# Kernel tuning notes

Hardware: AMD Instinct MI355X
Metric: run time of the kernel (lower is better)

Reference implementation:

```python
import jax, jax.numpy as jnp
import numpy as np

H_IN, W_IN = 512, 896          # input_shape
H, W = 64, 224                 # current_shape = (h, w_expand // 6)
N_CAM = 6
NPF = 256                      # num_pos_feats
TEMP = 10000.0


def setup_inputs():
    key = jax.random.key(0)
    k0, k1, k2, k3, k4, k5 = jax.random.split(key, 6)
    b, n = 8, N_CAM
    # extrinsic: 4x4 with a near-orthonormal rotation block and translation (cam height ~1.5m)
    rot = jnp.eye(3) + 0.1 * jax.random.normal(k0, (b, n, 3, 3), dtype=jnp.float32)
    trans = jax.random.normal(k1, (b, n, 3), dtype=jnp.float32)
    trans = trans.at[..., 2].set(1.5 + 0.1 * jnp.abs(trans[..., 2]))
    extrinsic = jnp.zeros((b, n, 4, 4), dtype=jnp.float32)
    extrinsic = extrinsic.at[:, :, :3, :3].set(rot)
    extrinsic = extrinsic.at[:, :, :3, 3].set(trans)
    extrinsic = extrinsic.at[:, :, 3, 3].set(1.0)
    # intrinsic: pinhole K = [[fx,0,cx],[0,fy,cy],[0,0,1]] (well conditioned, invertible)
    fx = 800.0 + 50.0 * jax.random.normal(k2, (b, n), dtype=jnp.float32)
    fy = 800.0 + 50.0 * jax.random.normal(k3, (b, n), dtype=jnp.float32)
    cx = jnp.full((b, n), W_IN / 2.0, dtype=jnp.float32)
    cy = jnp.full((b, n), H_IN / 2.0, dtype=jnp.float32)
    intrinsic = jnp.zeros((b, n, 3, 3), dtype=jnp.float32)
    intrinsic = intrinsic.at[:, :, 0, 0].set(fx).at[:, :, 1, 1].set(fy)
    intrinsic = intrinsic.at[:, :, 0, 2].set(cx).at[:, :, 1, 2].set(cy)
    intrinsic = intrinsic.at[:, :, 2, 2].set(1.0)
    # ida (image data augmentation) matrices: scale + shift affine, invertible
    s = 0.5 + 0.05 * jax.random.uniform(k4, (b, n), dtype=jnp.float32)
    t = 10.0 * jax.random.normal(k5, (b, n, 2), dtype=jnp.float32)
    ida = jnp.zeros((b, n, 3, 3), dtype=jnp.float32)
    ida = ida.at[:, :, 0, 0].set(s).at[:, :, 1, 1].set(s)
    ida = ida.at[:, :, 0, 2].set(t[..., 0]).at[:, :, 1, 2].set(t[..., 1])
    ida = ida.at[:, :, 2, 2].set(1.0)
    return {"extrinsic": extrinsic, "intrinsic": intrinsic, "ida_mats": ida, "do_flip": 0}


def reference(extrinsic, intrinsic, ida_mats, do_flip):
    b, n = extrinsic.shape[0], extrinsic.shape[1]
    # pixel grid over the full input image, sampled at feature resolution
    x = jnp.linspace(0.0, W_IN - 1, W, dtype=jnp.float32)
    y = jnp.linspace(0.0, H_IN - 1, H, dtype=jnp.float32)
    yg, xg = jnp.meshgrid(y, x, indexing="ij")            # (H, W)
    coords = jnp.stack([xg, yg, jnp.ones_like(xg)], -1)    # (H, W, 3) homogeneous
    # combined per-camera 3x3: R @ K^{-1} @ ida^{-1}
    M = jnp.einsum("bnij,bnjk->bnik", jnp.linalg.inv(intrinsic), jnp.linalg.inv(ida_mats))
    RM = jnp.einsum("bnij,bnjk->bnik", extrinsic[:, :, :3, :3], M)
    world = jnp.einsum("bnij,hwj->bnhwi", RM, coords)      # (b, n, H, W, 3)
    # F.normalize(p=2, dim=-1): x / max(||x||, eps)
    norm = jnp.maximum(jnp.linalg.norm(world, axis=-1, keepdims=True), 1e-12)
    world = world / norm
    z = world[..., 2]
    trans_z = extrinsic[:, :, 2, 3][:, :, None, None]      # (b, n, 1, 1)
    depth = -trans_z / z
    valid = (depth > 0)[..., None]                          # (b, n, H, W, 1)
    xy = world[..., :2] * depth[..., None]                  # (b, n, H, W, 2)
    if do_flip:
        xy = xy * jnp.array([1.0, -1.0], dtype=xy.dtype)
    # cat(unbind(dim=1), dim=-2): stitch cameras along width -> (b, H, n*W, ...)
    xy = jnp.transpose(xy, (0, 2, 1, 3, 4)).reshape(b, H, n * W, 2)
    valid = jnp.transpose(valid, (0, 2, 1, 3, 4)).reshape(b, H, n * W, 1)
    # sine encoding
    half = NPF // 2
    d = jnp.arange(half, dtype=jnp.float32)
    dim_t = TEMP ** (2.0 * jnp.floor(d / 2.0) / half)       # (half,)
    p = xy[..., None] / dim_t                               # (b, H, nW, 2, half)
    px = jnp.stack([jnp.sin(p[..., 0, 0::2]), jnp.cos(p[..., 0, 1::2])], -1).reshape(b, H, n * W, half)
    py = jnp.stack([jnp.sin(p[..., 1, 0::2]), jnp.cos(p[..., 1, 1::2])], -1).reshape(b, H, n * W, half)
    pos = jnp.concatenate([py, px], axis=-1)                # (b, H, nW, NPF)
    pos = jnp.where(valid, pos, jnp.float32(0.0))
    pos = jnp.transpose(pos, (0, 3, 1, 2))                  # (b, NPF, H, nW)
    return pos, valid[..., 0]
```

## Files before the change

### kernel.cpp

```cpp
#include <hip/hip_runtime.h>
#include <math.h>

namespace {
constexpr int B    = 8;
constexpr int NCAM = 6;
constexpr int H    = 64;
constexpr int W    = 224;
constexpr int NW   = NCAM * W;
constexpr int NPF  = 256;
constexpr int WP4  = NW / 4;
constexpr long long POS_ELEMS = (long long)B * NPF * H * NW;
}

__device__ __forceinline__ void inv3(const float m[9], float o[9]) {
  float a = m[0], b = m[1], c = m[2];
  float d = m[3], e = m[4], f = m[5];
  float g = m[6], h = m[7], i = m[8];
  float A  =  e * i - f * h;
  float Bm = -(d * i - f * g);
  float C  =  d * h - e * g;
  float det = a * A + b * Bm + c * C;
  float r = 1.0f / det;
  o[0] = A * r;  o[1] = -(b * i - c * h) * r; o[2] =  (b * f - c * e) * r;
  o[3] = Bm * r; o[4] =  (a * i - c * g) * r; o[5] = -(a * f - c * d) * r;
  o[6] = C * r;  o[7] = -(a * h - b * g) * r; o[8] =  (a * e - b * d) * r;
}

__device__ __forceinline__ void mm3(const float* a, const float* bm, float* o) {
#pragma unroll
  for (int i = 0; i < 3; ++i) {
#pragma unroll
    for (int j = 0; j < 3; ++j) {
      o[i * 3 + j] = fmaf(a[i * 3 + 0], bm[0 * 3 + j],
                     fmaf(a[i * 3 + 1], bm[1 * 3 + j],
                          a[i * 3 + 2] * bm[2 * 3 + j]));
    }
  }
}

__global__ __launch_bounds__(256) void ipm_pos_kernel(
    const float* __restrict__ ext, const float* __restrict__ intr,
    const float* __restrict__ ida, const int* __restrict__ do_flip,
    float* __restrict__ out, int write_valid) {
  const int t   = blockIdx.x * blockDim.x + threadIdx.x;
  const int wp4 = t % WP4;
  const int bh  = t / WP4;
  const int h   = bh % H;
  const int b   = bh / H;
  if (b >= B) return;
  const int wp0 = wp4 * 4;
  const int cam = wp0 / W;

  const int mi = b * NCAM + cam;
  const float* E  = ext  + mi * 16;
  const float* Km = intr + mi * 9;
  const float* Am = ida  + mi * 9;

  float R[9] = {E[0], E[1], E[2], E[4], E[5], E[6], E[8], E[9], E[10]};
  const float tz = E[11];
  float K[9], A[9];
#pragma unroll
  for (int i = 0; i < 9; ++i) { K[i] = Km[i]; A[i] = Am[i]; }

  float Ki[9], Ai[9], M[9], RM[9];
  inv3(K, Ki);
  inv3(A, Ai);
  mm3(Ki, Ai, M);
  mm3(R, M, RM);

  const float yp   = (float)h * (511.0f / 63.0f);
  const int   flip = *do_flip;

  float X[4], Y[4], vmask[4];
#pragma unroll
  for (int p = 0; p < 4; ++p) {
    const int w = wp0 + p - cam * W;
    const float xp = (float)w * (895.0f / 223.0f);
    float wx = fmaf(RM[0], xp, fmaf(RM[1], yp, RM[2]));
    float wy = fmaf(RM[3], xp, fmaf(RM[4], yp, RM[5]));
    float wz = fmaf(RM[6], xp, fmaf(RM[7], yp, RM[8]));
    float norm = sqrtf(wx * wx + wy * wy + wz * wz);
    norm = fmaxf(norm, 1e-12f);
    const float nz = wz / norm;
    const float depth = -tz / nz;
    const bool valid = depth > 0.0f;
    float Xp = (wx / norm) * depth;
    float Yp = (wy / norm) * depth;
    if (flip) Yp = -Yp;
    X[p] = valid ? Xp : 0.0f;
    Y[p] = valid ? Yp : 0.0f;
    vmask[p] = valid ? 1.0f : 0.0f;
  }
  const float amax = fmaxf(fmaxf(fabsf(X[0]), fabsf(X[1])),
                           fmaxf(fabsf(X[2]), fabsf(X[3])));
  const float amay = fmaxf(fmaxf(fabsf(Y[0]), fabsf(Y[1])),
                           fmaxf(fabsf(Y[2]), fabsf(Y[3])));
  const float ama  = fmaxf(amax, amay);

  const float c1     = 0.2076205059304498f;
  const float INV2PI = 0.15915494309189535f;
  const size_t cs  = (size_t)H * NW;
  const size_t o00 = ((size_t)b * NPF * H + h) * NW + wp0;

  for (int k = 0; k < 64; ++k) {
    const float inv_t = exp2f((float)(-k) * c1);
    float4 vsy, vcy, vsx, vcx;
    float sy[4], cy[4], sx[4], cx[4];
    if (__builtin_expect(!__any(ama * inv_t > 800.0f), 1)) {
      const float ck = inv_t * INV2PI;
#pragma unroll
      for (int p = 0; p < 4; ++p) {
        const float ry = Y[p] * ck;
        const float rx = X[p] * ck;
        sy[p] = __builtin_amdgcn_sinf(ry);
        cy[p] = __builtin_amdgcn_cosf(ry);
        sx[p] = __builtin_amdgcn_sinf(rx);
        cx[p] = __builtin_amdgcn_cosf(rx);
      }
    } else {
      const float tk = exp2f((float)k * c1);
#pragma unroll
      for (int p = 0; p < 4; ++p) {
        sincosf(Y[p] / tk, &sy[p], &cy[p]);
        sincosf(X[p] / tk, &sx[p], &cx[p]);
      }
    }
    vsy = make_float4(sy[0] * vmask[0], sy[1] * vmask[1], sy[2] * vmask[2], sy[3] * vmask[3]);
    vcy = make_float4(cy[0] * vmask[0], cy[1] * vmask[1], cy[2] * vmask[2], cy[3] * vmask[3]);
    vsx = make_float4(sx[0] * vmask[0], sx[1] * vmask[1], sx[2] * vmask[2], sx[3] * vmask[3]);
    vcx = make_float4(cx[0] * vmask[0], cx[1] * vmask[1], cx[2] * vmask[2], cx[3] * vmask[3]);

    const size_t o = o00 + (size_t)(2 * k) * cs;
    *(float4*)(out + o)            = vsy;
    *(float4*)(out + o + cs)       = vcy;
    *(float4*)(out + o + 128 * cs) = vsx;
    *(float4*)(out + o + 129 * cs) = vcx;
  }

  if (write_valid) {
    *(float4*)(out + POS_ELEMS + (size_t)bh * NW + wp0) =
        make_float4(vmask[0], vmask[1], vmask[2], vmask[3]);
  }
}

extern "C" void kernel_launch(void* const* d_in, const int* in_sizes, int n_in,
                              void* d_out, int out_size, void* d_ws, size_t ws_size,
                              hipStream_t stream) {
  const float* ext  = (const float*)d_in[0];
  const float* intr = (const float*)d_in[1];
  const float* ida  = (const float*)d_in[2];
  const int*   flip = (const int*)d_in[3];
  float* out = (float*)d_out;

  const int total = B * H * WP4 * 4 / 4;
  const int block = 256;
  const int grid  = (total + block - 1) / block;
  const int write_valid = ((long long)out_size > POS_ELEMS) ? 1 : 0;

  ipm_pos_kernel<<<grid, block, 0, stream>>>(ext, intr, ida, flip, out, write_valid);
}
```

Before: 689.7 us.

## Split into coordinate kernel and per-channel-plane sine encoding kernel

```diff
diff --git a/kernel.cpp b/kernel.cpp
--- a/kernel.cpp
+++ b/kernel.cpp
@@ -9,7 +9,12 @@
 constexpr int NW   = NCAM * W;
 constexpr int NPF  = 256;
 constexpr int WP4  = NW / 4;
-constexpr long long POS_ELEMS = (long long)B * NPF * H * NW;
+constexpr int NPIX = B * H * NW;
+constexpr int PLANE = H * NW;
+constexpr int PLANE4 = PLANE / 4;
+constexpr long long POS_ELEMS = (long long)B * NPF * (long long)PLANE;
+constexpr float C1     = 0.2076205059304498f;
+constexpr float INV2PI = 0.15915494309189535f;
 }
 
 __device__ __forceinline__ void inv3(const float m[9], float o[9]) {
@@ -28,20 +33,18 @@
 
 __device__ __forceinline__ void mm3(const float* a, const float* bm, float* o) {
 #pragma unroll
-  for (int i = 0; i < 3; ++i) {
+  for (int i = 0; i < 3; ++i)
 #pragma unroll
-    for (int j = 0; j < 3; ++j) {
+    for (int j = 0; j < 3; ++j)
       o[i * 3 + j] = fmaf(a[i * 3 + 0], bm[0 * 3 + j],
                      fmaf(a[i * 3 + 1], bm[1 * 3 + j],
                           a[i * 3 + 2] * bm[2 * 3 + j]));
-    }
-  }
 }
 
-__global__ __launch_bounds__(256) void ipm_pos_kernel(
+__global__ __launch_bounds__(256) void ipm_coords_kernel(
     const float* __restrict__ ext, const float* __restrict__ intr,
     const float* __restrict__ ida, const int* __restrict__ do_flip,
-    float* __restrict__ out, int write_valid) {
+    float* __restrict__ ws, float* __restrict__ out, int write_valid) {
   const int t   = blockIdx.x * blockDim.x + threadIdx.x;
   const int wp4 = t % WP4;
   const int bh  = t / WP4;
@@ -71,7 +74,7 @@
   const float yp   = (float)h * (511.0f / 63.0f);
   const int   flip = *do_flip;
 
-  float X[4], Y[4], vmask[4];
+  float X[4], Y[4], V[4];
 #pragma unroll
   for (int p = 0; p < 4; ++p) {
     const int w = wp0 + p - cam * W;
@@ -79,67 +82,80 @@
     float wx = fmaf(RM[0], xp, fmaf(RM[1], yp, RM[2]));
     float wy = fmaf(RM[3], xp, fmaf(RM[4], yp, RM[5]));
     float wz = fmaf(RM[6], xp, fmaf(RM[7], yp, RM[8]));
-    float norm = sqrtf(wx * wx + wy * wy + wz * wz);
-    norm = fmaxf(norm, 1e-12f);
-    const float nz = wz / norm;
-    const float depth = -tz / nz;
-    const bool valid = depth > 0.0f;
+    float norm = fmaxf(sqrtf(wx * wx + wy * wy + wz * wz), 1e-12f);
+    const float depth = -tz / (wz / norm);
+    const bool valid  = depth > 0.0f;
     float Xp = (wx / norm) * depth;
     float Yp = (wy / norm) * depth;
     if (flip) Yp = -Yp;
     X[p] = valid ? Xp : 0.0f;
     Y[p] = valid ? Yp : 0.0f;
-    vmask[p] = valid ? 1.0f : 0.0f;
+    V[p] = valid ? 1.0f : 0.0f;
   }
-  const float amax = fmaxf(fmaxf(fabsf(X[0]), fabsf(X[1])),
-                           fmaxf(fabsf(X[2]), fabsf(X[3])));
-  const float amay = fmaxf(fmaxf(fabsf(Y[0]), fabsf(Y[1])),
-                           fmaxf(fabsf(Y[2]), fabsf(Y[3])));
-  const float ama  = fmaxf(amax, amay);
 
-  const float c1     = 0.2076205059304498f;
-  const float INV2PI = 0.15915494309189535f;
-  const size_t cs  = (size_t)H * NW;
-  const size_t o00 = ((size_t)b * NPF * H + h) * NW + wp0;
+  const size_t o = (size_t)bh * NW + wp0;
+  *(float4*)(ws + o)            = make_float4(X[0], X[1], X[2], X[3]);
+  *(float4*)(ws + NPIX + o)     = make_float4(Y[0], Y[1], Y[2], Y[3]);
+  *(float4*)(ws + 2 * NPIX + o) = make_float4(V[0], V[1], V[2], V[3]);
+  if (write_valid)
+    *(float4*)(out + POS_ELEMS + o) = make_float4(V[0], V[1], V[2], V[3]);
+}
 
-  for (int k = 0; k < 64; ++k) {
-    const float inv_t = exp2f((float)(-k) * c1);
-    float4 vsy, vcy, vsx, vcx;
-    float sy[4], cy[4], sx[4], cx[4];
-    if (__builtin_expect(!__any(ama * inv_t > 800.0f), 1)) {
-      const float ck = inv_t * INV2PI;
-#pragma unroll
-      for (int p = 0; p < 4; ++p) {
-        const float ry = Y[p] * ck;
-        const float rx = X[p] * ck;
-        sy[p] = __builtin_amdgcn_sinf(ry);
-        cy[p] = __builtin_amdgcn_cosf(ry);
-        sx[p] = __builtin_amdgcn_sinf(rx);
-        cx[p] = __builtin_amdgcn_cosf(rx);
+__global__ __launch_bounds__(256) void ipm_encode_kernel(
+    const float* __restrict__ ws, float* __restrict__ out) {
+  const int blk = blockIdx.x;
+  const int id  = (blk & 7) * 256 + (blk >> 3);
+  const int b   = id >> 8;
+  const int c   = id & 255;
+
+  const bool isX   = c >= 128;
+  const int  k     = (c & 127) >> 1;
+  const bool isCos = (c & 1) != 0;
+
+  const float inv_t = exp2f(-(float)k * C1);
+  const float ck    = inv_t * INV2PI;
+
+  const float4* __restrict__ coord =
+      (const float4*)(ws + (isX ? 0 : NPIX) + (size_t)b * PLANE);
+  const float4* __restrict__ vmask =
+      (const float4*)(ws + 2 * NPIX + (size_t)b * PLANE);
+  float4* __restrict__ dst =
+      (float4*)(out + ((size_t)b * NPF + c) * PLANE);
+
+  const int tid = threadIdx.x;
+#pragma unroll 2
+  for (int i = tid; i < PLANE4; i += 256) {
+    const float4 v = coord[i];
+    const float am = fmaxf(fmaxf(fabsf(v.x), fabsf(v.y)),
+                           fmaxf(fabsf(v.z), fabsf(v.w)));
+    float4 r;
+    if (__builtin_expect(!__any(am * inv_t > 800.0f), 1)) {
+      if (isCos) {
+        r.x = __builtin_amdgcn_cosf(v.x * ck);
+        r.y = __builtin_amdgcn_cosf(v.y * ck);
+        r.z = __builtin_amdgcn_cosf(v.z * ck);
+        r.w = __builtin_amdgcn_cosf(v.w * ck);
+      } else {
+        r.x = __builtin_amdgcn_sinf(v.x * ck);
+        r.y = __builtin_amdgcn_sinf(v.y * ck);
+        r.z = __builtin_amdgcn_sinf(v.z * ck);
+        r.w = __builtin_amdgcn_sinf(v.w * ck);
       }
     } else {
-      const float tk = exp2f((float)k * c1);
-#pragma unroll
-      for (int p = 0; p < 4; ++p) {
-        sincosf(Y[p] / tk, &sy[p], &cy[p]);
-        sincosf(X[p] / tk, &sx[p], &cx[p]);
+      const float tk = exp2f((float)k * C1);
+      if (isCos) {
+        r.x = cosf(v.x / tk); r.y = cosf(v.y / tk);
+        r.z = cosf(v.z / tk); r.w = cosf(v.w / tk);
+      } else {
+        r.x = sinf(v.x / tk); r.y = sinf(v.y / tk);
+        r.z = sinf(v.z / tk); r.w = sinf(v.w / tk);
       }
     }
-    vsy = make_float4(sy[0] * vmask[0], sy[1] * vmask[1], sy[2] * vmask[2], sy[3] * vmask[3]);
-    vcy = make_float4(cy[0] * vmask[0], cy[1] * vmask[1], cy[2] * vmask[2], cy[3] * vmask[3]);
-    vsx = make_float4(sx[0] * vmask[0], sx[1] * vmask[1], sx[2] * vmask[2], sx[3] * vmask[3]);
-    vcx = make_float4(cx[0] * vmask[0], cx[1] * vmask[1], cx[2] * vmask[2], cx[3] * vmask[3]);
-
-    const size_t o = o00 + (size_t)(2 * k) * cs;
-    *(float4*)(out + o)            = vsy;
-    *(float4*)(out + o + cs)       = vcy;
-    *(float4*)(out + o + 128 * cs) = vsx;
-    *(float4*)(out + o + 129 * cs) = vcx;
-  }
-
-  if (write_valid) {
-    *(float4*)(out + POS_ELEMS + (size_t)bh * NW + wp0) =
-        make_float4(vmask[0], vmask[1], vmask[2], vmask[3]);
+    if (isCos) {
+      const float4 m = vmask[i];
+      r.x *= m.x; r.y *= m.y; r.z *= m.z; r.w *= m.w;
+    }
+    dst[i] = r;
   }
 }
 
@@ -151,11 +167,14 @@
   const float* ida  = (const float*)d_in[2];
   const int*   flip = (const int*)d_in[3];
   float* out = (float*)d_out;
+  float* ws  = (float*)d_ws;
 
-  const int total = B * H * WP4 * 4 / 4;
-  const int block = 256;
-  const int grid  = (total + block - 1) / block;
   const int write_valid = ((long long)out_size > POS_ELEMS) ? 1 : 0;
 
-  ipm_pos_kernel<<<grid, block, 0, stream>>>(ext, intr, ida, flip, out, write_valid);
+  const int grid1 = (B * H * WP4 + 255) / 256;
+  ipm_coords_kernel<<<grid1, 256, 0, stream>>>(ext, intr, ida, flip, ws, out,
+                                               write_valid);
+
+  const int grid2 = B * NPF;
+  ipm_encode_kernel<<<grid2, 256, 0, stream>>>(ws, out);
 }
```

New measurement: 743.2 us. 7.8% more time.
